# Kernel optimization log

Measured on AMD Instinct MI355X. Metric: run time of the kernel, lower is better.

Reference implementation:

```python
import jax, jax.numpy as jnp
import numpy as np

B, S, E, NH = 2, 2048, 1024, 4
DH = E // NH
EPS = 1e-6  # backend stabilization eps and layernorm eps


def setup_inputs() -> dict:
    key = jax.random.key(0)
    ks = jax.random.split(key, 7)
    q = jax.random.normal(ks[0], (B, S, E), jnp.float32)
    k = jax.random.normal(ks[1], (B, S, E), jnp.float32)
    v = jax.random.normal(ks[2], (B, S, E), jnp.float32)
    # Gate Dense layers: kernel zero-init in the module; use small random so the
    # math is non-trivial. Biases follow the module's inits.
    igate_kernel = 0.02 * jax.random.normal(ks[3], (3 * E, NH), jnp.float32)
    fgate_kernel = 0.02 * jax.random.normal(ks[4], (3 * E, NH), jnp.float32)
    igate_bias = 0.1 * jax.random.normal(ks[5], (NH,), jnp.float32)
    fgate_bias = jnp.linspace(3.0, 6.0, NH, dtype=jnp.float32)  # bias_linspace_init(3,6)
    outnorm_weight = jnp.ones((NH, DH), jnp.float32)
    return {
        "q": q, "k": k, "v": v,
        "igate_kernel": igate_kernel, "igate_bias": igate_bias,
        "fgate_kernel": fgate_kernel, "fgate_bias": fgate_bias,
        "outnorm_weight": outnorm_weight,
    }


def _mlstm_parallel_stabilized(q, k, v, ig, fg):
    # q,k,v: (B,NH,S,DH); ig,fg: (B,NH,S) gate pre-activations
    log_fg = jax.nn.log_sigmoid(fg)                     # (B,NH,S)
    c = jnp.cumsum(log_fg, axis=-1)                     # cumulative forget gates
    # log decay matrix: entry (i,j) = sum_{s=j+1..i} log_fg[s] = c[i]-c[j], causal
    log_fg_mat = c[..., :, None] - c[..., None, :]      # (B,NH,S,S)
    causal = jnp.tril(jnp.ones((S, S), bool))
    log_D = jnp.where(causal, log_fg_mat + ig[..., None, :], -jnp.inf)
    max_log_D = jnp.max(log_D, axis=-1, keepdims=True)  # (B,NH,S,1)
    D = jnp.exp(log_D - max_log_D)                      # stabilized decay matrix
    qk = jnp.einsum("bhsd,bhtd->bhst", q, k) / jnp.sqrt(jnp.float32(DH))
    C = qk * D                                          # (B,NH,S,S)
    normalizer = jnp.maximum(jnp.abs(jnp.sum(C, axis=-1, keepdims=True)),
                             jnp.exp(-max_log_D))
    C_norm = C / (normalizer + EPS)
    return jnp.einsum("bhst,bhtd->bhsd", C_norm, v)     # (B,NH,S,DH)


def reference(q, k, v, igate_kernel, igate_bias, fgate_kernel, fgate_bias, outnorm_weight):
    gate_in = jnp.concatenate([q, k, v], axis=-1)       # (B,S,3E)
    ig = gate_in @ igate_kernel + igate_bias            # (B,S,NH)
    fg = gate_in @ fgate_kernel + fgate_bias            # (B,S,NH)
    qh = q.reshape(B, S, NH, DH).transpose(0, 2, 1, 3)  # (B,NH,S,DH)
    kh = k.reshape(B, S, NH, DH).transpose(0, 2, 1, 3)
    vh = v.reshape(B, S, NH, DH).transpose(0, 2, 1, 3)
    h = _mlstm_parallel_stabilized(qh, kh, vh,
                                   ig.transpose(0, 2, 1), fg.transpose(0, 2, 1))
    h = h.transpose(0, 2, 1, 3)                          # (B,S,NH,DH)
    # MultiHeadLayerNorm: normalize over DH per head, weight only (no bias)
    mean = jnp.mean(h, axis=-1, keepdims=True)
    var = jnp.var(h, axis=-1, keepdims=True)
    h_norm = (h - mean) * jax.lax.rsqrt(var + EPS) * outnorm_weight
    return h_norm.reshape(B, S, E)
```

## Files before the change

### kernel.cpp

```cpp
#include <hip/hip_runtime.h>
#include <hip/hip_bf16.h>
#include <math.h>

#define B_  2
#define S_  2048
#define E_  1024
#define NH_ 4
#define DH_ 256
#define EPSF 1e-6f

typedef __attribute__((ext_vector_type(4)))  short  s16x4;
typedef __attribute__((ext_vector_type(8)))  short  s16x8;
typedef __attribute__((ext_vector_type(8)))  __bf16 bf16x8;
typedef __attribute__((ext_vector_type(4)))  float  f32x4;
typedef __attribute__((ext_vector_type(16))) float  f32x16;

static __device__ __forceinline__ short f2bf(float f) {
    unsigned u = __builtin_bit_cast(unsigned, f);
    u = (u + 0x7FFFu + ((u >> 16) & 1u)) >> 16;
    return (short)u;
}

static __device__ __forceinline__ void gload16(const void* g, void* l) {
    __builtin_amdgcn_global_load_lds(
        (__attribute__((address_space(1))) void*)g,
        (__attribute__((address_space(3))) void*)l, 16, 0, 0);
}

static __device__ __host__ __forceinline__ int chunk_prefix(int N) {
    int k = N >> 3, r = N & 7;
    return 4 * k * (k + 1) + r * (k + 1);
}

__global__ __launch_bounds__(256)
void prep_kernel(const float* __restrict__ q, const float* __restrict__ k,
                 const float* __restrict__ v,
                 const float* __restrict__ igk, const float* __restrict__ igb,
                 const float* __restrict__ fgk, const float* __restrict__ fgb,
                 short* __restrict__ qbf, short* __restrict__ kbf,
                 short* __restrict__ vt,
                 float* __restrict__ ig_ws, float* __restrict__ fg_ws) {
    const int bid = blockIdx.x;
    if (bid < 512) {
        int wid = threadIdx.x >> 6, lane = threadIdx.x & 63;
        int row0 = (bid * 4 + wid) * 2;
        int b = row0 >> 11;
        int s0 = row0 & 2047;
        float accI[2][4] = {};
        float accF[2][4] = {};
        const float* srcs[3] = {q, k, v};
        short* dsts[2] = {qbf, kbf};
#pragma unroll
        for (int p = 0; p < 3; p++) {
            const float* src = srcs[p] + ((long)b * S_ + s0) * E_;
#pragma unroll
            for (int c = 0; c < 4; c++) {
                int e = c * 256 + lane * 4;
                float4 x0 = *(const float4*)(src + e);
                float4 x1 = *(const float4*)(src + E_ + e);
                if (p < 2) {
                    s16x4 o0, o1;
                    o0[0] = f2bf(x0.x); o0[1] = f2bf(x0.y); o0[2] = f2bf(x0.z); o0[3] = f2bf(x0.w);
                    o1[0] = f2bf(x1.x); o1[1] = f2bf(x1.y); o1[2] = f2bf(x1.z); o1[3] = f2bf(x1.w);
                    long db = ((long)(b * NH_ + c) * S_ + s0) * DH_ + lane * 4;
                    *(s16x4*)(dsts[p] + db) = o0;
                    *(s16x4*)(dsts[p] + db + DH_) = o1;
                }
                const float4* wi = (const float4*)(igk + (long)(p * E_ + e) * 4);
                const float4* wf = (const float4*)(fgk + (long)(p * E_ + e) * 4);
                float xs0[4] = {x0.x, x0.y, x0.z, x0.w};
                float xs1[4] = {x1.x, x1.y, x1.z, x1.w};
#pragma unroll
                for (int j = 0; j < 4; j++) {
                    float4 wij = wi[j], wfj = wf[j];
                    accI[0][0] += xs0[j] * wij.x; accI[0][1] += xs0[j] * wij.y;
                    accI[0][2] += xs0[j] * wij.z; accI[0][3] += xs0[j] * wij.w;
                    accF[0][0] += xs0[j] * wfj.x; accF[0][1] += xs0[j] * wfj.y;
                    accF[0][2] += xs0[j] * wfj.z; accF[0][3] += xs0[j] * wfj.w;
                    accI[1][0] += xs1[j] * wij.x; accI[1][1] += xs1[j] * wij.y;
                    accI[1][2] += xs1[j] * wij.z; accI[1][3] += xs1[j] * wij.w;
                    accF[1][0] += xs1[j] * wfj.x; accF[1][1] += xs1[j] * wfj.y;
                    accF[1][2] += xs1[j] * wfj.z; accF[1][3] += xs1[j] * wfj.w;
                }
            }
        }
#pragma unroll
        for (int r = 0; r < 2; r++) {
#pragma unroll
            for (int hh = 0; hh < 4; hh++) {
                float aI = accI[r][hh], aF = accF[r][hh];
                for (int m = 1; m < 64; m <<= 1) { aI += __shfl_xor(aI, m); aF += __shfl_xor(aF, m); }
                if (lane == 0) {
                    ig_ws[((long)(b * NH_ + hh)) * S_ + s0 + r] = aI + igb[hh];
                    fg_ws[((long)(b * NH_ + hh)) * S_ + s0 + r] = aF + fgb[hh];
                }
            }
        }
    } else {
        __shared__ short tile[64][66];
        int b2 = bid - 512;
        int dt = b2 & 3, st = (b2 >> 2) & 31, hh = (b2 >> 7) & 3, b = b2 >> 9;
        int t = threadIdx.x;
#pragma unroll
        for (int rep = 0; rep < 16; rep++) {
            int idx = t + rep * 256;
            int ts = idx >> 6, td = idx & 63;
            float x = v[((long)b * S_ + st * 64 + ts) * E_ + hh * DH_ + dt * 64 + td];
            tile[ts][td] = f2bf(x);
        }
        __syncthreads();
        long obase = ((long)(b * NH_ + hh) * DH_ + dt * 64) * S_ + st * 64;
#pragma unroll
        for (int rep = 0; rep < 8; rep++) {
            int idx = t + rep * 256;
            int dd = idx >> 5, sp = (idx & 31) * 2;
            short2 val;
            val.x = tile[sp][dd];
            val.y = tile[sp + 1][dd];
            *(short2*)(vt + obase + (long)dd * S_ + sp) = val;
        }
    }
}

__global__ __launch_bounds__(256)
void scan_kernel(const float* __restrict__ ig_ws, const float* __restrict__ fg_ws,
                 float* __restrict__ c_ws, float* __restrict__ a_ws,
                 float* __restrict__ M_ws) {
    __shared__ float wsum[4], wmax[4];
    int seq = blockIdx.x;
    int tid = threadIdx.x, w = tid >> 6, lane = tid & 63;
    long base = (long)seq * S_;
    float carryC = 0.f, carryM = -INFINITY;
    for (int ch = 0; ch < S_ / 256; ch++) {
        int s = ch * 256 + tid;
        float fgv = fg_ws[base + s];
        float lf = (fgv > 0.f) ? -log1pf(expf(-fgv)) : (fgv - log1pf(expf(fgv)));
        float x = lf;
        for (int d = 1; d < 64; d <<= 1) { float t = __shfl_up(x, d); if (lane >= d) x += t; }
        if (lane == 63) wsum[w] = x;
        __syncthreads();
        float pre = carryC;
        for (int j = 0; j < w; j++) pre += wsum[j];
        float c = pre + x;
        float a = ig_ws[base + s] - c;
        float m = a;
        for (int d = 1; d < 64; d <<= 1) { float t = __shfl_up(m, d); if (lane >= d) m = fmaxf(m, t); }
        if (lane == 63) wmax[w] = m;
        __syncthreads();
        float prem = carryM;
        for (int j = 0; j < w; j++) prem = fmaxf(prem, wmax[j]);
        float M = fmaxf(prem, m);
        c_ws[base + s] = c;
        a_ws[base + s] = a;
        M_ws[base + s] = M;
        carryC += wsum[0] + wsum[1] + wsum[2] + wsum[3];
        carryM = fmaxf(fmaxf(fmaxf(carryM, wmax[0]), fmaxf(wmax[1], wmax[2])), wmax[3]);
        __syncthreads();
    }
}

__global__ __launch_bounds__(256)
void mlstm_sb1(const short* __restrict__ qbf, const short* __restrict__ kbf,
               const short* __restrict__ vt,
               const float* __restrict__ a_ws, const float* __restrict__ M_ws,
               float* __restrict__ num_ws, float* __restrict__ den_ws) {
    __shared__ __align__(16) char LDSb[73728];

    const int bid = blockIdx.x;
    const int seq = bid & 7;
    const int local = 79 - (bid >> 3);
    int qt = 0;
#pragma unroll
    for (int t = 1; t < 32; t++) if (chunk_prefix(t) <= local) qt = t;
    const int chunk = local - chunk_prefix(qt);
    const int kt0 = chunk * 8;
    const int kt1 = min(kt0 + 8, qt + 1);

    const int tid = threadIdx.x;
    const int w  = tid >> 6;
    const int rg = w & 1;
    const int ct = w >> 1;
    const int l  = tid & 63;
    const int l31 = l & 31;
    const int h5  = l >> 5;

    const long seqbase = (long)seq * S_ * DH_;
    const long gbase = (long)seq * S_;
    const int i0 = qt * 64;

    const char* kseq = (const char*)(kbf + seqbase);
    const char* vseq = (const char*)(vt + seqbase);

    int preK[8], preV[8];
#pragma unroll
    for (int i = 0; i < 8; i++) {
        int r = w * 16 + i * 2 + (l >> 5);
        preK[i] = r * 512 + (((l & 31) * 16) ^ ((r & 7) << 4));
        int d = w * 64 + i * 8 + (l >> 3);
        preV[i] = d * (S_ * 2) + (((l & 7) * 16) ^ ((d & 7) << 4));
    }

    float Mi[16];
#pragma unroll
    for (int reg = 0; reg < 16; reg++) {
        int rowL = 32 * rg + (reg & 3) + 8 * (reg >> 2) + 4 * h5;
        Mi[reg] = M_ws[gbase + i0 + rowL];
    }

#pragma unroll
    for (int rep = 0; rep < 8; rep++) {
        int idx = tid + rep * 256;
        int r = idx >> 5, c = idx & 31;
        s16x8 val = *(const s16x8*)(qbf + seqbase + (long)(i0 + r) * DH_ + c * 8);
        int byte = (r * 512 + c * 16) ^ ((r & 7) << 4);
        *(s16x8*)(LDSb + byte) = val;
    }
    __syncthreads();
    bf16x8 qfrag[16];
    {
        int qrow = 32 * rg + l31;
        int qswz = (qrow & 7) << 4;
#pragma unroll
        for (int dc = 0; dc < 16; dc++)
            qfrag[dc] = *(const bf16x8*)(LDSb + ((qrow * 512 + dc * 32 + h5 * 16) ^ qswz));
    }
    __syncthreads();

    f32x16 oacc[4] = {};
    float denacc[16] = {};

    const char* Klds  = LDSb;
    const char* Vtlds = LDSb + 32768;
    char* Plds = LDSb + 65536;

    for (int kt = kt0; kt < kt1; kt++) {
        const int j0 = kt * 64;

        {
            const char* ks = kseq + (long)j0 * 512;
            const char* vs = vseq + (long)j0 * 2;
            char* kd = LDSb + w * 8192;
            char* vd = LDSb + 32768 + w * 8192;
#pragma unroll
            for (int i = 0; i < 8; i++) gload16(ks + preK[i], kd + i * 1024);
#pragma unroll
            for (int i = 0; i < 8; i++) gload16(vs + preV[i], vd + i * 1024);
        }
        float aj = a_ws[gbase + j0 + 32 * ct + l31];
        __syncthreads();

        f32x16 sacc = {};
        {
            int j = 32 * ct + l31;
            int jswz = (j & 7) << 4;
            int jbase = j * 512;
#pragma unroll
            for (int dc = 0; dc < 16; dc++) {
                bf16x8 kf = *(const bf16x8*)(Klds + ((jbase + dc * 32 + h5 * 16) ^ jswz));
                sacc = __builtin_amdgcn_mfma_f32_32x32x16_bf16(qfrag[dc], kf, sacc, 0, 0, 0);
            }
        }

        {
            int jg = j0 + 32 * ct + l31;
#pragma unroll
            for (int reg = 0; reg < 16; reg++) {
                int rowL = 32 * rg + (reg & 3) + 8 * (reg >> 2) + 4 * h5;
                float p = sacc[reg] * 0.0625f * __expf(aj - Mi[reg]);
                if (jg > i0 + rowL) p = 0.f;
                denacc[reg] += p;
                int byte = (rowL * 128 + (32 * ct + l31) * 2) ^ ((rowL & 7) << 4);
                *(short*)(Plds + byte) = f2bf(p);
            }
        }
        __syncthreads();

        bf16x8 pfrag[4];
        {
            int prow = 32 * rg + l31;
            int pswz = (prow & 7) << 4;
#pragma unroll
            for (int k4 = 0; k4 < 4; k4++)
                pfrag[k4] = *(const bf16x8*)(Plds + ((prow * 128 + k4 * 32 + h5 * 16) ^ pswz));
        }
#pragma unroll
        for (int dt = 0; dt < 4; dt++) {
            int d = 128 * ct + 32 * dt + l31;
            int dbase = d * 128, dswz = (d & 7) << 4;
#pragma unroll
            for (int k4 = 0; k4 < 4; k4++) {
                bf16x8 vf = *(const bf16x8*)(Vtlds + ((dbase + k4 * 32 + h5 * 16) ^ dswz));
                oacc[dt] = __builtin_amdgcn_mfma_f32_32x32x16_bf16(pfrag[k4], vf, oacc[dt], 0, 0, 0);
            }
        }
        __syncthreads();
    }

    const long nbase = (long)bid * 64 * 256;
#pragma unroll
    for (int reg = 0; reg < 16; reg++) {
        float dsum = denacc[reg];
        dsum += __shfl_xor(dsum, 1);
        dsum += __shfl_xor(dsum, 2);
        dsum += __shfl_xor(dsum, 4);
        dsum += __shfl_xor(dsum, 8);
        dsum += __shfl_xor(dsum, 16);
        int rowL = 32 * rg + (reg & 3) + 8 * (reg >> 2) + 4 * h5;
        if (l31 == 0) den_ws[(long)bid * 128 + ct * 64 + rowL] = dsum;
    }
#pragma unroll
    for (int dt = 0; dt < 4; dt++) {
#pragma unroll
        for (int reg = 0; reg < 16; reg++) {
            int rowL = 32 * rg + (reg & 3) + 8 * (reg >> 2) + 4 * h5;
            num_ws[nbase + (long)rowL * 256 + 128 * ct + 32 * dt + l31] = oacc[dt][reg];
        }
    }
}

__global__ __launch_bounds__(256)
void reduce_kernel(const float* __restrict__ num_ws, const float* __restrict__ den_ws,
                   const float* __restrict__ c_ws, const float* __restrict__ M_ws,
                   const float* __restrict__ onw, float* __restrict__ out) {
    const int bid = blockIdx.x;
    const int seq = bid & 7;
    const int qh = bid >> 3;
    const int qt = qh >> 1;
    const int half = qh & 1;
    const int h = seq & 3;
    const int b = seq >> 2;
    const int nc = (qt >> 3) + 1;
    const int lbase = chunk_prefix(qt);
    const int w = threadIdx.x >> 6;
    const int l = threadIdx.x & 63;
    const long gbase = (long)seq * S_;

    float4 w4 = *(const float4*)(onw + h * DH_ + l * 4);

    for (int rr = 0; rr < 8; rr++) {
        int row = half * 32 + w * 8 + rr;
        int s = qt * 64 + row;
        float4 acc = {0.f, 0.f, 0.f, 0.f};
        float dsum = 0.f;
        for (int c = 0; c < nc; c++) {
            const long cid = (long)((79 - (lbase + c)) << 3) + seq;
            const float4 p = *(const float4*)(num_ws + cid * 16384 + (long)row * 256 + l * 4);
            acc.x += p.x; acc.y += p.y; acc.z += p.z; acc.w += p.w;
            dsum += den_ws[cid * 128 + row] + den_ws[cid * 128 + 64 + row];
        }
        float lb = __expf(-c_ws[gbase + s] - M_ws[gbase + s]);
        float inv = 1.f / (fmaxf(fabsf(dsum), lb) + EPSF);
        float4 x = {acc.x * inv, acc.y * inv, acc.z * inv, acc.w * inv};
        float sum = x.x + x.y + x.z + x.w;
        sum += __shfl_xor(sum, 1); sum += __shfl_xor(sum, 2); sum += __shfl_xor(sum, 4);
        sum += __shfl_xor(sum, 8); sum += __shfl_xor(sum, 16); sum += __shfl_xor(sum, 32);
        float mean = sum * (1.f / 256.f);
        float vx = x.x - mean, vy = x.y - mean, vz = x.z - mean, vw = x.w - mean;
        float vs = vx * vx + vy * vy + vz * vz + vw * vw;
        vs += __shfl_xor(vs, 1); vs += __shfl_xor(vs, 2); vs += __shfl_xor(vs, 4);
        vs += __shfl_xor(vs, 8); vs += __shfl_xor(vs, 16); vs += __shfl_xor(vs, 32);
        float rstd = rsqrtf(vs * (1.f / 256.f) + EPSF);
        float4 o;
        o.x = vx * rstd * w4.x; o.y = vy * rstd * w4.y;
        o.z = vz * rstd * w4.z; o.w = vw * rstd * w4.w;
        *(float4*)(out + ((long)b * S_ + s) * E_ + h * DH_ + l * 4) = o;
    }
}

__global__ __launch_bounds__(256)
void mlstm_mono(const short* __restrict__ qbf, const short* __restrict__ kbf,
                const short* __restrict__ vt,
                const float* __restrict__ a_ws, const float* __restrict__ M_ws,
                const float* __restrict__ c_ws, const float* __restrict__ onw,
                float* __restrict__ out) {
    __shared__ __align__(16) short Klds[64 * 256];
    __shared__ __align__(16) short Vtlds[256 * 64];
    short* Plds = Klds;

    const int bid = blockIdx.x;
    const int seq = bid & 7;
    const int qt = bid >> 3;
    const int h = seq & 3;
    const int b = seq >> 2;
    const int tid = threadIdx.x;
    const int w = tid >> 6;
    const int l = tid & 63;
    const int l15 = l & 15;
    const int g = l >> 4;

    const long seqbase = (long)seq * S_ * DH_;
    const long gbase = (long)seq * S_;
    const int i0 = qt * 64;

    float Mi_r[4], ci_r[4];
#pragma unroll
    for (int r = 0; r < 4; r++) {
        int il = 16 * w + 4 * g + r;
        Mi_r[r] = M_ws[gbase + i0 + il];
        ci_r[r] = c_ws[gbase + i0 + il];
    }
#pragma unroll
    for (int rep = 0; rep < 8; rep++) {
        int idx = tid + rep * 256;
        int r = idx >> 5, c = idx & 31;
        s16x8 val = *(const s16x8*)(qbf + seqbase + (long)(i0 + r) * DH_ + c * 8);
        int byte = (r * 512 + c * 16) ^ ((r & 7) << 4);
        *(s16x8*)((char*)Klds + byte) = val;
    }
    __syncthreads();
    bf16x8 qfrag[8];
#pragma unroll
    for (int dc = 0; dc < 8; dc++) {
        int r = 16 * w + l15;
        int byte = (r * 512 + (8 * g + 32 * dc) * 2) ^ ((r & 7) << 4);
        qfrag[dc] = *(const bf16x8*)((const char*)Klds + byte);
    }
    __syncthreads();

    const f32x4 fzero = {0.f, 0.f, 0.f, 0.f};
    f32x4 oacc[16];
#pragma unroll
    for (int dt = 0; dt < 16; dt++) oacc[dt] = fzero;
    float den[4] = {0.f, 0.f, 0.f, 0.f};

    const int nkt = qt + 1;
    for (int kt = 0; kt < nkt; kt++) {
        const int j0 = kt * 64;
#pragma unroll
        for (int rep = 0; rep < 8; rep++) {
            int idx = tid + rep * 256;
            int r = idx >> 5, c = idx & 31;
            s16x8 val = *(const s16x8*)(kbf + seqbase + (long)(j0 + r) * DH_ + c * 8);
            int byte = (r * 512 + c * 16) ^ ((r & 7) << 4);
            *(s16x8*)((char*)Klds + byte) = val;
        }
#pragma unroll
        for (int rep = 0; rep < 8; rep++) {
            int idx = tid + rep * 256;
            int d = idx >> 3, c = idx & 7;
            s16x8 val = *(const s16x8*)(vt + seqbase + (long)d * S_ + j0 + c * 8);
            int byte = (d * 128 + c * 16) ^ ((d & 7) << 4);
            *(s16x8*)((char*)Vtlds + byte) = val;
        }
        float aj_ct[4];
#pragma unroll
        for (int ct = 0; ct < 4; ct++) aj_ct[ct] = a_ws[gbase + j0 + 16 * ct + l15];
        __syncthreads();

        f32x4 sacc[4];
#pragma unroll
        for (int ct = 0; ct < 4; ct++) sacc[ct] = fzero;
#pragma unroll
        for (int dc = 0; dc < 8; dc++) {
#pragma unroll
            for (int ct = 0; ct < 4; ct++) {
                int j = 16 * ct + l15;
                int byte = (j * 512 + (8 * g + 32 * dc) * 2) ^ ((j & 7) << 4);
                bf16x8 kf = *(const bf16x8*)((const char*)Klds + byte);
                sacc[ct] = __builtin_amdgcn_mfma_f32_16x16x32_bf16(qfrag[dc], kf, sacc[ct], 0, 0, 0);
            }
        }
        __syncthreads();

        const bool diag = (kt == qt);
#pragma unroll
        for (int ct = 0; ct < 4; ct++) {
            int jl = 16 * ct + l15;
            float aj = aj_ct[ct];
#pragma unroll
            for (int r = 0; r < 4; r++) {
                int il = 16 * w + 4 * g + r;
                float p = sacc[ct][r] * 0.0625f * __expf(aj - Mi_r[r]);
                if (diag && jl > il) p = 0.f;
                den[r] += p;
                int byte = (il * 128 + jl * 2) ^ ((il & 7) << 4);
                *(short*)((char*)Plds + byte) = f2bf(p);
            }
        }
        __syncthreads();

        bf16x8 pfrag[2];
#pragma unroll
        for (int jc = 0; jc < 2; jc++) {
            int i = 16 * w + l15;
            int byte = (i * 128 + (8 * g + 32 * jc) * 2) ^ ((i & 7) << 4);
            pfrag[jc] = *(const bf16x8*)((const char*)Plds + byte);
        }
#pragma unroll
        for (int dt = 0; dt < 16; dt++) {
#pragma unroll
            for (int jc = 0; jc < 2; jc++) {
                int d = 16 * dt + l15;
                int byte = (d * 128 + (8 * g + 32 * jc) * 2) ^ ((d & 7) << 4);
                bf16x8 vf = *(const bf16x8*)((const char*)Vtlds + byte);
                oacc[dt] = __builtin_amdgcn_mfma_f32_16x16x32_bf16(pfrag[jc], vf, oacc[dt], 0, 0, 0);
            }
        }
        __syncthreads();
    }

#pragma unroll
    for (int r = 0; r < 4; r++) {
        float dsum = den[r];
        dsum += __shfl_xor(dsum, 1);
        dsum += __shfl_xor(dsum, 2);
        dsum += __shfl_xor(dsum, 4);
        dsum += __shfl_xor(dsum, 8);
        int il = 16 * w + 4 * g + r;
        float lb = __expf(-ci_r[r] - Mi_r[r]);
        float inv = 1.f / (fmaxf(fabsf(dsum), lb) + EPSF);
        float x[16];
        float sum = 0.f;
#pragma unroll
        for (int dt = 0; dt < 16; dt++) { x[dt] = oacc[dt][r] * inv; sum += x[dt]; }
        sum += __shfl_xor(sum, 1); sum += __shfl_xor(sum, 2);
        sum += __shfl_xor(sum, 4); sum += __shfl_xor(sum, 8);
        float mean = sum * (1.f / 256.f);
        float vs = 0.f;
#pragma unroll
        for (int dt = 0; dt < 16; dt++) { float dx = x[dt] - mean; vs += dx * dx; }
        vs += __shfl_xor(vs, 1); vs += __shfl_xor(vs, 2);
        vs += __shfl_xor(vs, 4); vs += __shfl_xor(vs, 8);
        float rstd = rsqrtf(vs * (1.f / 256.f) + EPSF);
        long orow = ((long)b * S_ + i0 + il) * E_ + h * DH_;
#pragma unroll
        for (int dt = 0; dt < 16; dt++) {
            int d = 16 * dt + l15;
            out[orow + d] = (x[dt] - mean) * rstd * onw[h * DH_ + d];
        }
    }
}

extern "C" void kernel_launch(void* const* d_in, const int* in_sizes, int n_in,
                              void* d_out, int out_size, void* d_ws, size_t ws_size,
                              hipStream_t stream) {
    const float* q   = (const float*)d_in[0];
    const float* k   = (const float*)d_in[1];
    const float* v   = (const float*)d_in[2];
    const float* igk = (const float*)d_in[3];
    const float* igb = (const float*)d_in[4];
    const float* fgk = (const float*)d_in[5];
    const float* fgb = (const float*)d_in[6];
    const float* onw = (const float*)d_in[7];
    float* out = (float*)d_out;

    char* ws = (char*)d_ws;
    float* ig_ws = (float*)(ws);
    float* fg_ws = (float*)(ws + (64  << 10));
    float* c_ws  = (float*)(ws + (128 << 10));
    float* a_ws  = (float*)(ws + (192 << 10));
    float* M_ws  = (float*)(ws + (256 << 10));
    short* qbf   = (short*)(ws + (1L  << 20));
    short* kbf   = (short*)(ws + (9L  << 20));
    short* vtb   = (short*)(ws + (17L << 20));
    float* num_ws = (float*)(ws + (25L << 20));
    float* den_ws = (float*)(ws + (65L << 20));

    prep_kernel<<<1536, 256, 0, stream>>>(q, k, v, igk, igb, fgk, fgb,
                                          qbf, kbf, vtb, ig_ws, fg_ws);
    scan_kernel<<<8, 256, 0, stream>>>(ig_ws, fg_ws, c_ws, a_ws, M_ws);

    if (ws_size >= (66L << 20)) {
        mlstm_sb1   <<<640, 256, 0, stream>>>(qbf, kbf, vtb, a_ws, M_ws, num_ws, den_ws);
        reduce_kernel<<<512, 256, 0, stream>>>(num_ws, den_ws, c_ws, M_ws, onw, out);
    } else {
        mlstm_mono  <<<256, 256, 0, stream>>>(qbf, kbf, vtb, a_ws, M_ws, c_ws, onw, out);
    }
}
```

Measured before the change: 148.7 us.

## Load K/V MFMA fragments directly from global memory into registers, bypassing LDS

```diff
diff --git a/kernel.cpp b/kernel.cpp
--- a/kernel.cpp
+++ b/kernel.cpp
@@ -19,12 +19,6 @@
     unsigned u = __builtin_bit_cast(unsigned, f);
     u = (u + 0x7FFFu + ((u >> 16) & 1u)) >> 16;
     return (short)u;
-}
-
-static __device__ __forceinline__ void gload16(const void* g, void* l) {
-    __builtin_amdgcn_global_load_lds(
-        (__attribute__((address_space(1))) void*)g,
-        (__attribute__((address_space(3))) void*)l, 16, 0, 0);
 }
 
 static __device__ __host__ __forceinline__ int chunk_prefix(int N) {
@@ -160,11 +154,11 @@
 }
 
 __global__ __launch_bounds__(256)
-void mlstm_sb1(const short* __restrict__ qbf, const short* __restrict__ kbf,
+void mlstm_reg(const short* __restrict__ qbf, const short* __restrict__ kbf,
                const short* __restrict__ vt,
                const float* __restrict__ a_ws, const float* __restrict__ M_ws,
                float* __restrict__ num_ws, float* __restrict__ den_ws) {
-    __shared__ __align__(16) char LDSb[73728];
+    __shared__ __align__(16) char Plds[8192];
 
     const int bid = blockIdx.x;
     const int seq = bid & 7;
@@ -188,16 +182,12 @@
     const long gbase = (long)seq * S_;
     const int i0 = qt * 64;
 
-    const char* kseq = (const char*)(kbf + seqbase);
-    const char* vseq = (const char*)(vt + seqbase);
-
-    int preK[8], preV[8];
-#pragma unroll
-    for (int i = 0; i < 8; i++) {
-        int r = w * 16 + i * 2 + (l >> 5);
-        preK[i] = r * 512 + (((l & 31) * 16) ^ ((r & 7) << 4));
-        int d = w * 64 + i * 8 + (l >> 3);
-        preV[i] = d * (S_ * 2) + (((l & 7) * 16) ^ ((d & 7) << 4));
+    bf16x8 qfrag[16];
+    {
+        const short* qp = qbf + seqbase + (long)(i0 + 32 * rg + l31) * DH_ + h5 * 8;
+#pragma unroll
+        for (int dc = 0; dc < 16; dc++)
+            qfrag[dc] = *(const bf16x8*)(qp + dc * 16);
     }
 
     float Mi[16];
@@ -207,58 +197,27 @@
         Mi[reg] = M_ws[gbase + i0 + rowL];
     }
 
-#pragma unroll
-    for (int rep = 0; rep < 8; rep++) {
-        int idx = tid + rep * 256;
-        int r = idx >> 5, c = idx & 31;
-        s16x8 val = *(const s16x8*)(qbf + seqbase + (long)(i0 + r) * DH_ + c * 8);
-        int byte = (r * 512 + c * 16) ^ ((r & 7) << 4);
-        *(s16x8*)(LDSb + byte) = val;
-    }
-    __syncthreads();
-    bf16x8 qfrag[16];
-    {
-        int qrow = 32 * rg + l31;
-        int qswz = (qrow & 7) << 4;
-#pragma unroll
-        for (int dc = 0; dc < 16; dc++)
-            qfrag[dc] = *(const bf16x8*)(LDSb + ((qrow * 512 + dc * 32 + h5 * 16) ^ qswz));
-    }
-    __syncthreads();
-
     f32x16 oacc[4] = {};
     float denacc[16] = {};
 
-    const char* Klds  = LDSb;
-    const char* Vtlds = LDSb + 32768;
-    char* Plds = LDSb + 65536;
-
     for (int kt = kt0; kt < kt1; kt++) {
         const int j0 = kt * 64;
-
-        {
-            const char* ks = kseq + (long)j0 * 512;
-            const char* vs = vseq + (long)j0 * 2;
-            char* kd = LDSb + w * 8192;
-            char* vd = LDSb + 32768 + w * 8192;
-#pragma unroll
-            for (int i = 0; i < 8; i++) gload16(ks + preK[i], kd + i * 1024);
-#pragma unroll
-            for (int i = 0; i < 8; i++) gload16(vs + preV[i], vd + i * 1024);
-        }
         float aj = a_ws[gbase + j0 + 32 * ct + l31];
-        __syncthreads();
 
         f32x16 sacc = {};
         {
-            int j = 32 * ct + l31;
-            int jswz = (j & 7) << 4;
-            int jbase = j * 512;
-#pragma unroll
-            for (int dc = 0; dc < 16; dc++) {
-                bf16x8 kf = *(const bf16x8*)(Klds + ((jbase + dc * 32 + h5 * 16) ^ jswz));
-                sacc = __builtin_amdgcn_mfma_f32_32x32x16_bf16(qfrag[dc], kf, sacc, 0, 0, 0);
-            }
+            const short* kp = kbf + seqbase + (long)(j0 + 32 * ct + l31) * DH_ + h5 * 8;
+            bf16x8 kr0[8], kr1[8];
+#pragma unroll
+            for (int dc = 0; dc < 8; dc++) kr0[dc] = *(const bf16x8*)(kp + dc * 16);
+#pragma unroll
+            for (int dc = 0; dc < 8; dc++)
+                sacc = __builtin_amdgcn_mfma_f32_32x32x16_bf16(qfrag[dc], kr0[dc], sacc, 0, 0, 0);
+#pragma unroll
+            for (int dc = 0; dc < 8; dc++) kr1[dc] = *(const bf16x8*)(kp + (dc + 8) * 16);
+#pragma unroll
+            for (int dc = 0; dc < 8; dc++)
+                sacc = __builtin_amdgcn_mfma_f32_32x32x16_bf16(qfrag[dc + 8], kr1[dc], sacc, 0, 0, 0);
         }
 
         {
@@ -273,7 +232,8 @@
                 *(short*)(Plds + byte) = f2bf(p);
             }
         }
-        __syncthreads();
+        asm volatile("s_waitcnt lgkmcnt(0)" ::: "memory");
+        __builtin_amdgcn_s_barrier();
 
         bf16x8 pfrag[4];
         {
@@ -286,14 +246,16 @@
 #pragma unroll
         for (int dt = 0; dt < 4; dt++) {
             int d = 128 * ct + 32 * dt + l31;
-            int dbase = d * 128, dswz = (d & 7) << 4;
-#pragma unroll
-            for (int k4 = 0; k4 < 4; k4++) {
-                bf16x8 vf = *(const bf16x8*)(Vtlds + ((dbase + k4 * 32 + h5 * 16) ^ dswz));
-                oacc[dt] = __builtin_amdgcn_mfma_f32_32x32x16_bf16(pfrag[k4], vf, oacc[dt], 0, 0, 0);
-            }
-        }
-        __syncthreads();
+            const short* vp = vt + seqbase + (long)d * S_ + j0 + h5 * 8;
+            bf16x8 vr[4];
+#pragma unroll
+            for (int k4 = 0; k4 < 4; k4++) vr[k4] = *(const bf16x8*)(vp + k4 * 16);
+#pragma unroll
+            for (int k4 = 0; k4 < 4; k4++)
+                oacc[dt] = __builtin_amdgcn_mfma_f32_32x32x16_bf16(pfrag[k4], vr[k4], oacc[dt], 0, 0, 0);
+        }
+        asm volatile("s_waitcnt lgkmcnt(0)" ::: "memory");
+        __builtin_amdgcn_s_barrier();
     }
 
     const long nbase = (long)bid * 64 * 256;
@@ -561,7 +523,7 @@
     scan_kernel<<<8, 256, 0, stream>>>(ig_ws, fg_ws, c_ws, a_ws, M_ws);
 
     if (ws_size >= (66L << 20)) {
-        mlstm_sb1   <<<640, 256, 0, stream>>>(qbf, kbf, vtb, a_ws, M_ws, num_ws, den_ws);
+        mlstm_reg   <<<640, 256, 0, stream>>>(qbf, kbf, vtb, a_ws, M_ws, num_ws, den_ws);
         reduce_kernel<<<512, 256, 0, stream>>>(num_ws, den_ws, c_ws, M_ws, onw, out);
     } else {
         mlstm_mono  <<<256, 256, 0, stream>>>(qbf, kbf, vtb, a_ws, M_ws, c_ws, onw, out);
```

After: 198.1 us. 1.33x slower.

## Rebalance split-K: split only long query tiles in two, finalize short tiles in-kernel

Applied to the files above, without the earlier changes.

```diff
diff --git a/kernel.cpp b/kernel.cpp
--- a/kernel.cpp
+++ b/kernel.cpp
@@ -25,11 +25,6 @@
     __builtin_amdgcn_global_load_lds(
         (__attribute__((address_space(1))) void*)g,
         (__attribute__((address_space(3))) void*)l, 16, 0, 0);
-}
-
-static __device__ __host__ __forceinline__ int chunk_prefix(int N) {
-    int k = N >> 3, r = N & 7;
-    return 4 * k * (k + 1) + r * (k + 1);
 }
 
 __global__ __launch_bounds__(256)
@@ -122,17 +117,17 @@
     }
 }
 
-__global__ __launch_bounds__(256)
+__global__ __launch_bounds__(1024)
 void scan_kernel(const float* __restrict__ ig_ws, const float* __restrict__ fg_ws,
                  float* __restrict__ c_ws, float* __restrict__ a_ws,
                  float* __restrict__ M_ws) {
-    __shared__ float wsum[4], wmax[4];
+    __shared__ float wsum[16], wmax[16];
     int seq = blockIdx.x;
     int tid = threadIdx.x, w = tid >> 6, lane = tid & 63;
     long base = (long)seq * S_;
     float carryC = 0.f, carryM = -INFINITY;
-    for (int ch = 0; ch < S_ / 256; ch++) {
-        int s = ch * 256 + tid;
+    for (int ch = 0; ch < S_ / 1024; ch++) {
+        int s = ch * 1024 + tid;
         float fgv = fg_ws[base + s];
         float lf = (fgv > 0.f) ? -log1pf(expf(-fgv)) : (fgv - log1pf(expf(fgv)));
         float x = lf;
@@ -153,8 +148,10 @@
         c_ws[base + s] = c;
         a_ws[base + s] = a;
         M_ws[base + s] = M;
-        carryC += wsum[0] + wsum[1] + wsum[2] + wsum[3];
-        carryM = fmaxf(fmaxf(fmaxf(carryM, wmax[0]), fmaxf(wmax[1], wmax[2])), wmax[3]);
+        float allsum = 0.f, allmax = -INFINITY;
+        for (int j = 0; j < 16; j++) { allsum += wsum[j]; allmax = fmaxf(allmax, wmax[j]); }
+        carryC += allsum;
+        carryM = fmaxf(carryM, allmax);
         __syncthreads();
     }
 }
@@ -163,18 +160,29 @@
 void mlstm_sb1(const short* __restrict__ qbf, const short* __restrict__ kbf,
                const short* __restrict__ vt,
                const float* __restrict__ a_ws, const float* __restrict__ M_ws,
-               float* __restrict__ num_ws, float* __restrict__ den_ws) {
+               const float* __restrict__ c_ws, const float* __restrict__ onw,
+               float* __restrict__ num_ws, float* __restrict__ den_ws,
+               float* __restrict__ out) {
     __shared__ __align__(16) char LDSb[73728];
 
     const int bid = blockIdx.x;
     const int seq = bid & 7;
-    const int local = 79 - (bid >> 3);
-    int qt = 0;
-#pragma unroll
-    for (int t = 1; t < 32; t++) if (chunk_prefix(t) <= local) qt = t;
-    const int chunk = local - chunk_prefix(qt);
-    const int kt0 = chunk * 8;
-    const int kt1 = min(kt0 + 8, qt + 1);
+    const int local = bid >> 3;
+    int qt, kt0, kt1, pq;
+    bool direct;
+    if (local < 32) {
+        qt = 31 - (local >> 1);
+        int nkt = qt + 1;
+        int c0 = (nkt + 1) >> 1;
+        if ((local & 1) == 0) { kt0 = 0; kt1 = c0; } else { kt0 = c0; kt1 = nkt; }
+        pq = (qt - 16) * 2 + (local & 1);
+        direct = false;
+    } else {
+        qt = 47 - local;
+        kt0 = 0; kt1 = qt + 1;
+        pq = 0;
+        direct = true;
+    }
 
     const int tid = threadIdx.x;
     const int w  = tid >> 6;
@@ -183,6 +191,8 @@
     const int l  = tid & 63;
     const int l31 = l & 31;
     const int h5  = l >> 5;
+    const int h = seq & 3;
+    const int b = seq >> 2;
 
     const long seqbase = (long)seq * S_ * DH_;
     const long gbase = (long)seq * S_;
@@ -200,11 +210,12 @@
         preV[i] = d * (S_ * 2) + (((l & 7) * 16) ^ ((d & 7) << 4));
     }
 
-    float Mi[16];
+    float Mi[16], ci[16];
 #pragma unroll
     for (int reg = 0; reg < 16; reg++) {
         int rowL = 32 * rg + (reg & 3) + 8 * (reg >> 2) + 4 * h5;
         Mi[reg] = M_ws[gbase + i0 + rowL];
+        ci[reg] = c_ws[gbase + i0 + rowL];
     }
 
 #pragma unroll
@@ -235,7 +246,6 @@
 
     for (int kt = kt0; kt < kt1; kt++) {
         const int j0 = kt * 64;
-
         {
             const char* ks = kseq + (long)j0 * 512;
             const char* vs = vseq + (long)j0 * 2;
@@ -260,7 +270,6 @@
                 sacc = __builtin_amdgcn_mfma_f32_32x32x16_bf16(qfrag[dc], kf, sacc, 0, 0, 0);
             }
         }
-
         {
             int jg = j0 + 32 * ct + l31;
 #pragma unroll
@@ -296,7 +305,7 @@
         __syncthreads();
     }
 
-    const long nbase = (long)bid * 64 * 256;
+    float dred[16];
 #pragma unroll
     for (int reg = 0; reg < 16; reg++) {
         float dsum = denacc[reg];
@@ -305,15 +314,82 @@
         dsum += __shfl_xor(dsum, 4);
         dsum += __shfl_xor(dsum, 8);
         dsum += __shfl_xor(dsum, 16);
-        int rowL = 32 * rg + (reg & 3) + 8 * (reg >> 2) + 4 * h5;
-        if (l31 == 0) den_ws[(long)bid * 128 + ct * 64 + rowL] = dsum;
-    }
-#pragma unroll
-    for (int dt = 0; dt < 4; dt++) {
+        dred[reg] = dsum;
+    }
+
+    if (!direct) {
+        const long cid = (long)pq * 8 + seq;
+        const long nbase = cid * 64 * 256;
 #pragma unroll
         for (int reg = 0; reg < 16; reg++) {
             int rowL = 32 * rg + (reg & 3) + 8 * (reg >> 2) + 4 * h5;
-            num_ws[nbase + (long)rowL * 256 + 128 * ct + 32 * dt + l31] = oacc[dt][reg];
+            if (l31 == 0) den_ws[cid * 128 + ct * 64 + rowL] = dred[reg];
+        }
+#pragma unroll
+        for (int dt = 0; dt < 4; dt++) {
+#pragma unroll
+            for (int reg = 0; reg < 16; reg++) {
+                int rowL = 32 * rg + (reg & 3) + 8 * (reg >> 2) + 4 * h5;
+                num_ws[nbase + (long)rowL * 256 + 128 * ct + 32 * dt + l31] = oacc[dt][reg];
+            }
+        }
+        return;
+    }
+
+    float* fl = (float*)Plds;
+#pragma unroll
+    for (int reg = 0; reg < 16; reg++) {
+        int rowL = 32 * rg + (reg & 3) + 8 * (reg >> 2) + 4 * h5;
+        if (l31 == 0) fl[rowL * 2 + ct] = dred[reg];
+    }
+    __syncthreads();
+    float inv[16];
+#pragma unroll
+    for (int reg = 0; reg < 16; reg++) {
+        int rowL = 32 * rg + (reg & 3) + 8 * (reg >> 2) + 4 * h5;
+        float den = fl[rowL * 2] + fl[rowL * 2 + 1];
+        float lb = __expf(-ci[reg] - Mi[reg]);
+        inv[reg] = 1.f / (fmaxf(fabsf(den), lb) + EPSF);
+    }
+#pragma unroll
+    for (int reg = 0; reg < 16; reg++) {
+        float s = 0.f;
+#pragma unroll
+        for (int dt = 0; dt < 4; dt++) { oacc[dt][reg] *= inv[reg]; s += oacc[dt][reg]; }
+        s += __shfl_xor(s, 1); s += __shfl_xor(s, 2); s += __shfl_xor(s, 4);
+        s += __shfl_xor(s, 8); s += __shfl_xor(s, 16);
+        int rowL = 32 * rg + (reg & 3) + 8 * (reg >> 2) + 4 * h5;
+        if (l31 == 0) fl[128 + rowL * 2 + ct] = s;
+    }
+    __syncthreads();
+    float mean[16];
+#pragma unroll
+    for (int reg = 0; reg < 16; reg++) {
+        int rowL = 32 * rg + (reg & 3) + 8 * (reg >> 2) + 4 * h5;
+        mean[reg] = (fl[128 + rowL * 2] + fl[128 + rowL * 2 + 1]) * (1.f / 256.f);
+    }
+#pragma unroll
+    for (int reg = 0; reg < 16; reg++) {
+        float vs = 0.f;
+#pragma unroll
+        for (int dt = 0; dt < 4; dt++) { float dx = oacc[dt][reg] - mean[reg]; vs += dx * dx; }
+        vs += __shfl_xor(vs, 1); vs += __shfl_xor(vs, 2); vs += __shfl_xor(vs, 4);
+        vs += __shfl_xor(vs, 8); vs += __shfl_xor(vs, 16);
+        int rowL = 32 * rg + (reg & 3) + 8 * (reg >> 2) + 4 * h5;
+        if (l31 == 0) fl[256 + rowL * 2 + ct] = vs;
+    }
+    __syncthreads();
+#pragma unroll
+    for (int dt = 0; dt < 4; dt++) {
+        int dcol = 128 * ct + 32 * dt + l31;
+        float wv = onw[h * DH_ + dcol];
+#pragma unroll
+        for (int reg = 0; reg < 16; reg++) {
+            int rowL = 32 * rg + (reg & 3) + 8 * (reg >> 2) + 4 * h5;
+            float var = (fl[256 + rowL * 2] + fl[256 + rowL * 2 + 1]) * (1.f / 256.f);
+            float rstd = rsqrtf(var + EPSF);
+            out[((long)b * S_ + i0 + rowL) * E_ + h * DH_ + dcol] =
+                (oacc[dt][reg] - mean[reg]) * rstd * wv;
         }
     }
 }
@@ -325,29 +401,26 @@
     const int bid = blockIdx.x;
     const int seq = bid & 7;
     const int qh = bid >> 3;
-    const int qt = qh >> 1;
+    const int qt = 16 + (qh >> 1);
     const int half = qh & 1;
     const int h = seq & 3;
     const int b = seq >> 2;
-    const int nc = (qt >> 3) + 1;
-    const int lbase = chunk_prefix(qt);
     const int w = threadIdx.x >> 6;
     const int l = threadIdx.x & 63;
     const long gbase = (long)seq * S_;
+    const long cid0 = (long)((qt - 16) * 2) * 8 + seq;
+    const long cid1 = cid0 + 8;
 
     float4 w4 = *(const float4*)(onw + h * DH_ + l * 4);
 
     for (int rr = 0; rr < 8; rr++) {
         int row = half * 32 + w * 8 + rr;
         int s = qt * 64 + row;
-        float4 acc = {0.f, 0.f, 0.f, 0.f};
-        float dsum = 0.f;
-        for (int c = 0; c < nc; c++) {
-            const long cid = (long)((79 - (lbase + c)) << 3) + seq;
-            const float4 p = *(const float4*)(num_ws + cid * 16384 + (long)row * 256 + l * 4);
-            acc.x += p.x; acc.y += p.y; acc.z += p.z; acc.w += p.w;
-            dsum += den_ws[cid * 128 + row] + den_ws[cid * 128 + 64 + row];
-        }
+        const float4 p0 = *(const float4*)(num_ws + cid0 * 16384 + (long)row * 256 + l * 4);
+        const float4 p1 = *(const float4*)(num_ws + cid1 * 16384 + (long)row * 256 + l * 4);
+        float4 acc = {p0.x + p1.x, p0.y + p1.y, p0.z + p1.z, p0.w + p1.w};
+        float dsum = den_ws[cid0 * 128 + row] + den_ws[cid0 * 128 + 64 + row]
+                   + den_ws[cid1 * 128 + row] + den_ws[cid1 * 128 + 64 + row];
         float lb = __expf(-c_ws[gbase + s] - M_ws[gbase + s]);
         float inv = 1.f / (fmaxf(fabsf(dsum), lb) + EPSF);
         float4 x = {acc.x * inv, acc.y * inv, acc.z * inv, acc.w * inv};
@@ -554,15 +627,16 @@
     short* kbf   = (short*)(ws + (9L  << 20));
     short* vtb   = (short*)(ws + (17L << 20));
     float* num_ws = (float*)(ws + (25L << 20));
-    float* den_ws = (float*)(ws + (65L << 20));
+    float* den_ws = (float*)(ws + (60L << 20));
 
     prep_kernel<<<1536, 256, 0, stream>>>(q, k, v, igk, igb, fgk, fgb,
                                           qbf, kbf, vtb, ig_ws, fg_ws);
-    scan_kernel<<<8, 256, 0, stream>>>(ig_ws, fg_ws, c_ws, a_ws, M_ws);
-
-    if (ws_size >= (66L << 20)) {
-        mlstm_sb1   <<<640, 256, 0, stream>>>(qbf, kbf, vtb, a_ws, M_ws, num_ws, den_ws);
-        reduce_kernel<<<512, 256, 0, stream>>>(num_ws, den_ws, c_ws, M_ws, onw, out);
+    scan_kernel<<<8, 1024, 0, stream>>>(ig_ws, fg_ws, c_ws, a_ws, M_ws);
+
+    if (ws_size >= (61L << 20)) {
+        mlstm_sb1   <<<384, 256, 0, stream>>>(qbf, kbf, vtb, a_ws, M_ws, c_ws, onw,
+                                              num_ws, den_ws, out);
+        reduce_kernel<<<256, 256, 0, stream>>>(num_ws, den_ws, c_ws, M_ws, onw, out);
     } else {
         mlstm_mono  <<<256, 256, 0, stream>>>(qbf, kbf, vtb, a_ws, M_ws, c_ws, onw, out);
     }
```

Result: faster. 130.8 us, median of 2 (-12.0%).
